# Performance work log

Hardware: AMD Instinct MI355X
Metric: run time of the kernel (lower is better)

The kernel has to match this reference:

```python
import jax, jax.numpy as jnp
import numpy as np


def setup_inputs() -> dict:
    key = jax.random.key(0)
    ks = jax.random.split(key, 7)
    B, S, H = 16, 512, 768
    NS = 4096
    MAX_W = 10
    WDIM = 150
    NL = 25
    hidden_states = jax.random.normal(ks[0], (B, S, H), dtype=jnp.float32)
    spans = jax.random.randint(ks[1], (B, NS, 3), 0, MAX_W + 1, dtype=jnp.int64)
    width_emb = jax.random.normal(ks[2], (MAX_W + 1, WDIM), dtype=jnp.float32) * 0.02
    in_dim = 2 * H + WDIM
    W1 = jax.random.normal(ks[3], (in_dim, H), dtype=jnp.float32) / np.sqrt(in_dim)
    b1 = jnp.zeros((H,), dtype=jnp.float32)
    W2 = jax.random.normal(ks[4], (H, NL), dtype=jnp.float32) / np.sqrt(H)
    b2 = jnp.zeros((NL,), dtype=jnp.float32)
    return {"hidden_states": hidden_states, "spans": spans,
            "width_emb": width_emb, "W1": W1, "b1": b1, "W2": W2, "b2": b2}


def reference(hidden_states, spans, width_emb, W1, b1, W2, b2):
    # batched_index_select(one-hot @ bmm) == gather along seq dim
    starts = spans[:, :, 0]            # [B, NS]
    ends = spans[:, :, 1]              # [B, NS]
    widths = spans[:, :, 2]            # [B, NS]
    start_emb = jnp.take_along_axis(hidden_states, starts[:, :, None], axis=1)  # [B,NS,H]
    end_emb = jnp.take_along_axis(hidden_states, ends[:, :, None], axis=1)      # [B,NS,H]
    w_emb = width_emb[widths]          # [B, NS, WDIM]
    span_emb = jnp.concatenate([start_emb, end_emb, w_emb], axis=-1)  # [B,NS,2H+WDIM]
    h = jax.nn.relu(jnp.einsum('bnd,dh->bnh', span_emb, W1) + b1)
    logits = jnp.einsum('bnh,hl->bnl', h, W2) + b2
    return logits
```

## Files before the change

### kernel.cpp

```cpp
#include <hip/hip_runtime.h>
#include <hip/hip_bf16.h>


#define NB 16
#define NH 768
#define NV 11
#define NL 25
#define NCOMBO 1331

typedef __attribute__((ext_vector_type(8))) short frag8;
typedef __attribute__((ext_vector_type(4))) float f32x4;

__device__ __forceinline__ unsigned short f2bf(float f) {
    unsigned int u = __float_as_uint(f);
    u = (u + 0x7FFFu + ((u >> 16) & 1u)) >> 16;
    return (unsigned short)u;
}
__device__ __forceinline__ unsigned int pack2(float lo, float hi) {
    return (unsigned int)f2bf(lo) | ((unsigned int)f2bf(hi) << 16);
}


#define TST 68
__global__ __launch_bounds__(256) void prep_kernel(
    const float* __restrict__ hs, const float* __restrict__ W1,
    const float* __restrict__ W2, const float* __restrict__ wemb,
    unsigned short* __restrict__ W1F, unsigned short* __restrict__ W2F,
    unsigned short* __restrict__ HSA, float* __restrict__ PW)
{
    __shared__ float T[64 * TST];
    const int x = blockIdx.x, y = blockIdx.y, tid = threadIdx.x;

    if (x < 24) {
        const int k0 = x * 64, n0 = y * 64;
        #pragma unroll
        for (int p = 0; p < 4; ++p) {
            int kl = (tid >> 4) + p * 16;
            int n4 = tid & 15;
            *(float4*)&T[kl * TST + n4 * 4] =
                *(const float4*)&W1[(size_t)(k0 + kl) * NH + n0 + n4 * 4];
        }
        __syncthreads();
        const int n = tid >> 2, kgl = tid & 3;
        const int nt = y * 4 + (n >> 4), ln = n & 15;
        #pragma unroll
        for (int half = 0; half < 2; ++half) {
            const int kk = kgl * 16 + half * 8;
            unsigned int o[4];
            #pragma unroll
            for (int i = 0; i < 4; ++i) {
                float a = T[(kk + 2 * i) * TST + n];
                float b = T[(kk + 2 * i + 1) * TST + n];
                o[i] = pack2(a, b);
            }
            const int kg = x * 2 + (kk >> 5);
            const int q = (kk >> 3) & 3;
            *(uint4*)&W1F[((((size_t)nt * 48 + kg) * 16 + ln) * 4 + q) * 8] =
                make_uint4(o[0], o[1], o[2], o[3]);
        }
    } else if (x == 24) {
        const int kcl = tid >> 7, nt = (tid >> 6) & 1, ln = (tid >> 2) & 15, q = tid & 3;
        const int n2 = nt * 16 + ln;
        const int k = y * 64 + kcl * 32 + q * 8;
        unsigned int o[4];
        #pragma unroll
        for (int i = 0; i < 4; ++i) {
            float a = (n2 < NL) ? W2[(size_t)(k + 2 * i) * NL + n2] : 0.0f;
            float b = (n2 < NL) ? W2[(size_t)(k + 2 * i + 1) * NL + n2] : 0.0f;
            o[i] = pack2(a, b);
        }
        *(uint4*)&W2F[((((size_t)(y * 2 + kcl)) * 2 + nt) * 16 + ln) * 32 + q * 8] =
            make_uint4(o[0], o[1], o[2], o[3]);
    } else if (x == 25) {
        const int n = y * 64 + (tid & 63);
        const int vg = tid >> 6;
        float acc[3] = {0.f, 0.f, 0.f};
        for (int k = 0; k < 150; k += 2) {
            float w1a = W1[(size_t)(1536 + k) * NH + n];
            float w1b = W1[(size_t)(1537 + k) * NH + n];
            #pragma unroll
            for (int j = 0; j < 3; ++j) {
                int v = vg + j * 4; int vs = (v < NV) ? v : 0;
                acc[j] += wemb[vs * 150 + k] * w1a + wemb[vs * 150 + k + 1] * w1b;
            }
        }
        #pragma unroll
        for (int j = 0; j < 3; ++j) {
            int v = vg + j * 4;
            if (v < NV) PW[(size_t)v * NH + n] = acc[j];
        }
    } else {
        const int mt = y;
        #pragma unroll
        for (int it = 0; it < 6; ++it) {
            int u = it * 256 + tid;
            int kc = u >> 6, ln = (u >> 2) & 15, q = u & 3;
            int m = mt * 16 + ln;
            int b = m / 12, v = m - 12 * b;
            unsigned int o[4] = {0, 0, 0, 0};
            if (v < NV) {
                const float* p = hs + ((size_t)(b * 512 + v)) * NH + kc * 32 + q * 8;
                float4 a = *(const float4*)p;
                float4 c = *(const float4*)(p + 4);
                o[0] = pack2(a.x, a.y); o[1] = pack2(a.z, a.w);
                o[2] = pack2(c.x, c.y); o[3] = pack2(c.z, c.w);
            }
            *(uint4*)&HSA[((((size_t)mt * 24 + kc) * 16 + ln) * 4 + q) * 8] =
                make_uint4(o[0], o[1], o[2], o[3]);
        }
    }
}

__global__ __launch_bounds__(256) void precompute_kernel(
    const unsigned short* __restrict__ HSA, const unsigned short* __restrict__ W1F,
    const float* __restrict__ b1,
    float* __restrict__ PS, float* __restrict__ PE)
{
    const int tid = threadIdx.x;
    const int wave = tid >> 6, lane = tid & 63, q = lane >> 4, ln = lane & 15;
    const int job = blockIdx.x * 4 + wave;
    const int part = job >= 576;
    const int j2 = job - part * 576;
    const int nt = j2 / 12;
    const int mt = j2 - nt * 12;

    const unsigned short* aP = HSA + (size_t)mt * 24 * 512 + ln * 32 + q * 8;
    const unsigned short* bP = W1F + ((size_t)nt * 48 + part * 24) * 512 + ln * 32 + q * 8;

    f32x4 acc;
    #pragma unroll
    for (int r = 0; r < 4; ++r) acc[r] = 0.0f;

    #pragma unroll 6
    for (int kc = 0; kc < 24; ++kc) {
        frag8 aF = *(const frag8*)(aP + kc * 512);
        frag8 bF = *(const frag8*)(bP + kc * 512);
        acc = __builtin_amdgcn_mfma_f32_16x16x32_bf16(aF, bF, acc, 0, 0, 0);
    }

    float* dst = part ? PE : PS;
    const int n = nt * 16 + ln;
    const float bb = part ? 0.0f : b1[n];
    #pragma unroll
    for (int r = 0; r < 4; ++r) {
        int m = mt * 16 + q * 4 + r;
        int b = m / 12, v = m - 12 * b;
        if (v < NV)
            dst[((size_t)(b * NV + v)) * NH + n] = acc[r] + bb;
    }
}

#define PFST 388
__global__ __launch_bounds__(256) void combo_kernel(
    const float* __restrict__ PS, const float* __restrict__ PE,
    const float* __restrict__ PW, const unsigned short* __restrict__ W2F,
    float* __restrict__ LT)
{
    __shared__ float baseL[384];
    __shared__ float peL[NV * PFST];
    __shared__ float pwL[NV * PFST];

    const int tid = threadIdx.x;
    const int wave = tid >> 6, lane = tid & 63, q = lane >> 4, ln = lane & 15;
    const int b = blockIdx.x / NV, s = blockIdx.x - NV * b;
    const int kb = blockIdx.y * 384;

    const float* ps = PS + (size_t)(b * NV + s) * NH + kb;
    for (int i = tid; i < 96; i += 256)
        *(float4*)&baseL[i * 4] = *(const float4*)&ps[i * 4];
    for (int i = tid; i < NV * 96; i += 256) {
        int v = i / 96, j = i - 96 * v;
        *(float4*)&peL[v * PFST + j * 4] =
            *(const float4*)&PE[((size_t)(b * NV + v)) * NH + kb + j * 4];
        *(float4*)&pwL[v * PFST + j * 4] =
            *(const float4*)&PW[(size_t)v * NH + kb + j * 4];
    }

    int eIdx[2], wIdx[2];
    #pragma unroll
    for (int mtl = 0; mtl < 2; ++mtl) {
        int m = (wave * 2 + mtl) * 16 + ln;
        int me = (m < 121) ? m : 120;
        eIdx[mtl] = (me * 373) >> 12;
        wIdx[mtl] = me - NV * eIdx[mtl];
    }

    f32x4 acc[2][2];
    #pragma unroll
    for (int a = 0; a < 2; ++a)
        #pragma unroll
        for (int c = 0; c < 2; ++c)
            #pragma unroll
            for (int r = 0; r < 4; ++r) acc[a][c][r] = 0.0f;

    const unsigned short* w2p = W2F + ((size_t)blockIdx.y * 12) * 1024 + ln * 32 + q * 8;

    __syncthreads();

    for (int ch = 0; ch < 6; ++ch) {
        #pragma unroll
        for (int kt = 0; kt < 2; ++kt) {
            const int kk = ch * 64 + kt * 32 + q * 8;
            float4 c0 = *(const float4*)&baseL[kk];
            float4 c1 = *(const float4*)&baseL[kk + 4];
            frag8 af[2];
            #pragma unroll
            for (int mtl = 0; mtl < 2; ++mtl) {
                const float* pe = &peL[eIdx[mtl] * PFST + kk];
                const float* pw = &pwL[wIdx[mtl] * PFST + kk];
                float4 p0 = *(const float4*)pe, p1 = *(const float4*)(pe + 4);
                float4 w0 = *(const float4*)pw, w1 = *(const float4*)(pw + 4);
                union { uint4 u; frag8 f; } cv;
                cv.u = make_uint4(
                    pack2(fmaxf(c0.x + p0.x + w0.x, 0.f), fmaxf(c0.y + p0.y + w0.y, 0.f)),
                    pack2(fmaxf(c0.z + p0.z + w0.z, 0.f), fmaxf(c0.w + p0.w + w0.w, 0.f)),
                    pack2(fmaxf(c1.x + p1.x + w1.x, 0.f), fmaxf(c1.y + p1.y + w1.y, 0.f)),
                    pack2(fmaxf(c1.z + p1.z + w1.z, 0.f), fmaxf(c1.w + p1.w + w1.w, 0.f)));
                af[mtl] = cv.f;
            }
            #pragma unroll
            for (int nt = 0; nt < 2; ++nt) {
                frag8 bf = *(const frag8*)(w2p + ((ch * 2 + kt) * 2 + nt) * 512);
                #pragma unroll
                for (int mtl = 0; mtl < 2; ++mtl)
                    acc[mtl][nt] = __builtin_amdgcn_mfma_f32_16x16x32_bf16(
                        af[mtl], bf, acc[mtl][nt], 0, 0, 0);
            }
        }
    }

    float* LTz = LT + (size_t)blockIdx.y * (NB * NCOMBO * NL);
    #pragma unroll
    for (int nt = 0; nt < 2; ++nt) {
        int n = nt * 16 + ln;
        if (n < NL) {
            #pragma unroll
            for (int mtl = 0; mtl < 2; ++mtl)
                #pragma unroll
                for (int r = 0; r < 4; ++r) {
                    int m = (wave * 2 + mtl) * 16 + q * 4 + r;
                    if (m < 121)
                        LTz[((size_t)b * NCOMBO + s * 121 + m) * NL + n] =
                            acc[mtl][nt][r];
                }
        }
    }
}

__global__ __launch_bounds__(256) void gather_kernel(
    const int* __restrict__ spans, const float* __restrict__ LT,
    const float* __restrict__ b2, float* __restrict__ out)
{
    const int idx = blockIdx.x * 256 + threadIdx.x;
    const int span = idx / NL;
    const int c = idx - span * NL;
    const int b = span >> 12;
    const int s = spans[span * 3 + 0];
    const int e = spans[span * 3 + 1];
    const int w = spans[span * 3 + 2];
    const size_t cidx = (size_t)(b * NCOMBO + s * 121 + e * NV + w) * NL + c;
    out[idx] = LT[cidx] + LT[(size_t)NB * NCOMBO * NL + cidx] + b2[c];
}

extern "C" void kernel_launch(void* const* d_in, const int* in_sizes, int n_in,
                              void* d_out, int out_size, void* d_ws, size_t ws_size,
                              hipStream_t stream) {
    const float* hs    = (const float*)d_in[0];
    const int*   spans = (const int*)d_in[1];
    const float* wemb  = (const float*)d_in[2];
    const float* W1    = (const float*)d_in[3];
    const float* b1    = (const float*)d_in[4];
    const float* W2    = (const float*)d_in[5];
    const float* b2    = (const float*)d_in[6];
    float* out = (float*)d_out;

    float* PS = (float*)d_ws;
    float* PE = PS + NB * NV * NH;
    float* PW = PE + NB * NV * NH;
    float* LT = PW + NV * NH;
    unsigned short* W1F = (unsigned short*)(LT + 2 * NB * NCOMBO * NL);
    unsigned short* W2F = W1F + (size_t)48 * 48 * 512;
    unsigned short* HSA = W2F + (size_t)24 * 2 * 512;

    prep_kernel<<<dim3(27, 12), dim3(256), 0, stream>>>(
        hs, W1, W2, wemb, W1F, W2F, HSA, PW);
    precompute_kernel<<<dim3(288), dim3(256), 0, stream>>>(HSA, W1F, b1, PS, PE);
    combo_kernel<<<dim3(NB * NV, 2), dim3(256), 0, stream>>>(PS, PE, PW, W2F, LT);
    gather_kernel<<<dim3((NB * 4096 * NL) / 256), dim3(256), 0, stream>>>(
        spans, LT, b2, out);
}
```

Baseline: 119.2 us.

## Fuse four stage kernels into one cooperative persistent kernel with grid syncs

Merges the prep, precompute, combo and gather kernels into a single cooperative kernel with 256 blocks. Each stage loops over its former grid as jobs, and grid-wide syncs separate the stages. Shared memory is unioned between the transpose tile and the combo buffers. The aim is to remove three kernel launch gaps and their tail effects. In exchange it pays grid-sync costs, and each stage now runs with fewer blocks than before, which may reduce parallelism for the gather and combo phases.

```diff
diff --git a/kernel.cpp b/kernel.cpp
--- a/kernel.cpp
+++ b/kernel.cpp
@@ -1,5 +1,8 @@
 #include <hip/hip_runtime.h>
 #include <hip/hip_bf16.h>
+#include <hip/hip_cooperative_groups.h>
+
+namespace cg = cooperative_groups;
 
 
 #define NB 16
@@ -20,246 +23,252 @@
     return (unsigned int)f2bf(lo) | ((unsigned int)f2bf(hi) << 16);
 }
 
-
 #define TST 68
-__global__ __launch_bounds__(256) void prep_kernel(
-    const float* __restrict__ hs, const float* __restrict__ W1,
-    const float* __restrict__ W2, const float* __restrict__ wemb,
-    unsigned short* __restrict__ W1F, unsigned short* __restrict__ W2F,
-    unsigned short* __restrict__ HSA, float* __restrict__ PW)
+#define PFST 388
+
+__global__ __launch_bounds__(256) void fused_kernel(
+    const float* __restrict__ hs, const int* __restrict__ spans,
+    const float* __restrict__ wemb, const float* __restrict__ W1,
+    const float* __restrict__ b1, const float* __restrict__ W2,
+    const float* __restrict__ b2, float* __restrict__ out,
+    float* __restrict__ PS, float* __restrict__ PE, float* __restrict__ PW,
+    float* __restrict__ LT, unsigned short* __restrict__ W1F,
+    unsigned short* __restrict__ W2F, unsigned short* __restrict__ HSA)
 {
-    __shared__ float T[64 * TST];
-    const int x = blockIdx.x, y = blockIdx.y, tid = threadIdx.x;
-
-    if (x < 24) {
-        const int k0 = x * 64, n0 = y * 64;
-        #pragma unroll
-        for (int p = 0; p < 4; ++p) {
-            int kl = (tid >> 4) + p * 16;
-            int n4 = tid & 15;
-            *(float4*)&T[kl * TST + n4 * 4] =
-                *(const float4*)&W1[(size_t)(k0 + kl) * NH + n0 + n4 * 4];
-        }
-        __syncthreads();
-        const int n = tid >> 2, kgl = tid & 3;
-        const int nt = y * 4 + (n >> 4), ln = n & 15;
-        #pragma unroll
-        for (int half = 0; half < 2; ++half) {
-            const int kk = kgl * 16 + half * 8;
-            unsigned int o[4];
-            #pragma unroll
-            for (int i = 0; i < 4; ++i) {
-                float a = T[(kk + 2 * i) * TST + n];
-                float b = T[(kk + 2 * i + 1) * TST + n];
-                o[i] = pack2(a, b);
-            }
-            const int kg = x * 2 + (kk >> 5);
-            const int q = (kk >> 3) & 3;
-            *(uint4*)&W1F[((((size_t)nt * 48 + kg) * 16 + ln) * 4 + q) * 8] =
-                make_uint4(o[0], o[1], o[2], o[3]);
-        }
-    } else if (x == 24) {
-        const int kcl = tid >> 7, nt = (tid >> 6) & 1, ln = (tid >> 2) & 15, q = tid & 3;
-        const int n2 = nt * 16 + ln;
-        const int k = y * 64 + kcl * 32 + q * 8;
-        unsigned int o[4];
-        #pragma unroll
-        for (int i = 0; i < 4; ++i) {
-            float a = (n2 < NL) ? W2[(size_t)(k + 2 * i) * NL + n2] : 0.0f;
-            float b = (n2 < NL) ? W2[(size_t)(k + 2 * i + 1) * NL + n2] : 0.0f;
-            o[i] = pack2(a, b);
-        }
-        *(uint4*)&W2F[((((size_t)(y * 2 + kcl)) * 2 + nt) * 16 + ln) * 32 + q * 8] =
-            make_uint4(o[0], o[1], o[2], o[3]);
-    } else if (x == 25) {
-        const int n = y * 64 + (tid & 63);
-        const int vg = tid >> 6;
-        float acc[3] = {0.f, 0.f, 0.f};
-        for (int k = 0; k < 150; k += 2) {
-            float w1a = W1[(size_t)(1536 + k) * NH + n];
-            float w1b = W1[(size_t)(1537 + k) * NH + n];
-            #pragma unroll
-            for (int j = 0; j < 3; ++j) {
-                int v = vg + j * 4; int vs = (v < NV) ? v : 0;
-                acc[j] += wemb[vs * 150 + k] * w1a + wemb[vs * 150 + k + 1] * w1b;
-            }
-        }
-        #pragma unroll
-        for (int j = 0; j < 3; ++j) {
-            int v = vg + j * 4;
-            if (v < NV) PW[(size_t)v * NH + n] = acc[j];
-        }
-    } else {
-        const int mt = y;
-        #pragma unroll
-        for (int it = 0; it < 6; ++it) {
-            int u = it * 256 + tid;
-            int kc = u >> 6, ln = (u >> 2) & 15, q = u & 3;
-            int m = mt * 16 + ln;
-            int b = m / 12, v = m - 12 * b;
-            unsigned int o[4] = {0, 0, 0, 0};
-            if (v < NV) {
-                const float* p = hs + ((size_t)(b * 512 + v)) * NH + kc * 32 + q * 8;
-                float4 a = *(const float4*)p;
-                float4 c = *(const float4*)(p + 4);
-                o[0] = pack2(a.x, a.y); o[1] = pack2(a.z, a.w);
-                o[2] = pack2(c.x, c.y); o[3] = pack2(c.z, c.w);
-            }
-            *(uint4*)&HSA[((((size_t)mt * 24 + kc) * 16 + ln) * 4 + q) * 8] =
-                make_uint4(o[0], o[1], o[2], o[3]);
-        }
-    }
-}
-
-__global__ __launch_bounds__(256) void precompute_kernel(
-    const unsigned short* __restrict__ HSA, const unsigned short* __restrict__ W1F,
-    const float* __restrict__ b1,
-    float* __restrict__ PS, float* __restrict__ PE)
-{
+    __shared__ union {
+        float T[64 * TST];
+        struct {
+            float baseL[384];
+            float peL[NV * PFST];
+            float pwL[NV * PFST];
+        } c;
+    } sm;
+
+    cg::grid_group grid = cg::this_grid();
     const int tid = threadIdx.x;
     const int wave = tid >> 6, lane = tid & 63, q = lane >> 4, ln = lane & 15;
-    const int job = blockIdx.x * 4 + wave;
-    const int part = job >= 576;
-    const int j2 = job - part * 576;
-    const int nt = j2 / 12;
-    const int mt = j2 - nt * 12;
-
-    const unsigned short* aP = HSA + (size_t)mt * 24 * 512 + ln * 32 + q * 8;
-    const unsigned short* bP = W1F + ((size_t)nt * 48 + part * 24) * 512 + ln * 32 + q * 8;
-
-    f32x4 acc;
-    #pragma unroll
-    for (int r = 0; r < 4; ++r) acc[r] = 0.0f;
-
-    #pragma unroll 6
-    for (int kc = 0; kc < 24; ++kc) {
-        frag8 aF = *(const frag8*)(aP + kc * 512);
-        frag8 bF = *(const frag8*)(bP + kc * 512);
-        acc = __builtin_amdgcn_mfma_f32_16x16x32_bf16(aF, bF, acc, 0, 0, 0);
+
+    for (int job = blockIdx.x; job < 324; job += 256) {
+        const int x = job / 12, y = job - x * 12;
+        if (x < 24) {
+            const int k0 = x * 64, n0 = y * 64;
+            #pragma unroll
+            for (int p = 0; p < 4; ++p) {
+                int kl = (tid >> 4) + p * 16;
+                int n4 = tid & 15;
+                *(float4*)&sm.T[kl * TST + n4 * 4] =
+                    *(const float4*)&W1[(size_t)(k0 + kl) * NH + n0 + n4 * 4];
+            }
+            __syncthreads();
+            const int n = tid >> 2, kgl = tid & 3;
+            const int nt = y * 4 + (n >> 4), lnn = n & 15;
+            #pragma unroll
+            for (int half = 0; half < 2; ++half) {
+                const int kk = kgl * 16 + half * 8;
+                unsigned int o[4];
+                #pragma unroll
+                for (int i = 0; i < 4; ++i) {
+                    float a = sm.T[(kk + 2 * i) * TST + n];
+                    float bv = sm.T[(kk + 2 * i + 1) * TST + n];
+                    o[i] = pack2(a, bv);
+                }
+                const int kg = x * 2 + (kk >> 5);
+                const int qq = (kk >> 3) & 3;
+                *(uint4*)&W1F[((((size_t)nt * 48 + kg) * 16 + lnn) * 4 + qq) * 8] =
+                    make_uint4(o[0], o[1], o[2], o[3]);
+            }
+            __syncthreads();
+        } else if (x == 24) {
+            const int kcl = tid >> 7, ntl = (tid >> 6) & 1,
+                      lnl = (tid >> 2) & 15, ql = tid & 3;
+            const int n2 = ntl * 16 + lnl;
+            const int k = y * 64 + kcl * 32 + ql * 8;
+            unsigned int o[4];
+            #pragma unroll
+            for (int i = 0; i < 4; ++i) {
+                float a = (n2 < NL) ? W2[(size_t)(k + 2 * i) * NL + n2] : 0.0f;
+                float bv = (n2 < NL) ? W2[(size_t)(k + 2 * i + 1) * NL + n2] : 0.0f;
+                o[i] = pack2(a, bv);
+            }
+            *(uint4*)&W2F[((((size_t)(y * 2 + kcl)) * 2 + ntl) * 16 + lnl) * 32 + ql * 8] =
+                make_uint4(o[0], o[1], o[2], o[3]);
+        } else if (x == 25) {
+            const int n = y * 64 + (tid & 63);
+            const int vg = tid >> 6;
+            float acc[3] = {0.f, 0.f, 0.f};
+            for (int k = 0; k < 150; k += 2) {
+                float w1a = W1[(size_t)(1536 + k) * NH + n];
+                float w1b = W1[(size_t)(1537 + k) * NH + n];
+                #pragma unroll
+                for (int j = 0; j < 3; ++j) {
+                    int v = vg + j * 4; int vs = (v < NV) ? v : 0;
+                    acc[j] += wemb[vs * 150 + k] * w1a + wemb[vs * 150 + k + 1] * w1b;
+                }
+            }
+            #pragma unroll
+            for (int j = 0; j < 3; ++j) {
+                int v = vg + j * 4;
+                if (v < NV) PW[(size_t)v * NH + n] = acc[j];
+            }
+        } else {
+            const int mt = y;
+            #pragma unroll
+            for (int it = 0; it < 6; ++it) {
+                int u = it * 256 + tid;
+                int kc = u >> 6, lnl = (u >> 2) & 15, ql = u & 3;
+                int m = mt * 16 + lnl;
+                int b = m / 12, v = m - 12 * b;
+                unsigned int o[4] = {0, 0, 0, 0};
+                if (v < NV) {
+                    const float* p = hs + ((size_t)(b * 512 + v)) * NH + kc * 32 + ql * 8;
+                    float4 a = *(const float4*)p;
+                    float4 c = *(const float4*)(p + 4);
+                    o[0] = pack2(a.x, a.y); o[1] = pack2(a.z, a.w);
+                    o[2] = pack2(c.x, c.y); o[3] = pack2(c.z, c.w);
+                }
+                *(uint4*)&HSA[((((size_t)mt * 24 + kc) * 16 + lnl) * 4 + ql) * 8] =
+                    make_uint4(o[0], o[1], o[2], o[3]);
+            }
+        }
     }
 
-    float* dst = part ? PE : PS;
-    const int n = nt * 16 + ln;
-    const float bb = part ? 0.0f : b1[n];
-    #pragma unroll
-    for (int r = 0; r < 4; ++r) {
-        int m = mt * 16 + q * 4 + r;
-        int b = m / 12, v = m - 12 * b;
-        if (v < NV)
-            dst[((size_t)(b * NV + v)) * NH + n] = acc[r] + bb;
+    grid.sync();
+
+    for (int job = blockIdx.x * 4 + wave; job < 1152; job += 1024) {
+        const int part = job >= 576;
+        const int j2 = job - part * 576;
+        const int nt = j2 / 12;
+        const int mt = j2 - nt * 12;
+
+        const unsigned short* aP = HSA + (size_t)mt * 24 * 512 + ln * 32 + q * 8;
+        const unsigned short* bP = W1F + ((size_t)nt * 48 + part * 24) * 512 + ln * 32 + q * 8;
+
+        f32x4 acc;
+        #pragma unroll
+        for (int r = 0; r < 4; ++r) acc[r] = 0.0f;
+        #pragma unroll 6
+        for (int kc = 0; kc < 24; ++kc) {
+            frag8 aF = *(const frag8*)(aP + kc * 512);
+            frag8 bF = *(const frag8*)(bP + kc * 512);
+            acc = __builtin_amdgcn_mfma_f32_16x16x32_bf16(aF, bF, acc, 0, 0, 0);
+        }
+
+        float* dst = part ? PE : PS;
+        const int n = nt * 16 + ln;
+        const float bb = part ? 0.0f : b1[n];
+        #pragma unroll
+        for (int r = 0; r < 4; ++r) {
+            int m = mt * 16 + q * 4 + r;
+            int b = m / 12, v = m - 12 * b;
+            if (v < NV)
+                dst[((size_t)(b * NV + v)) * NH + n] = acc[r] + bb;
+        }
     }
-}
-
-#define PFST 388
-__global__ __launch_bounds__(256) void combo_kernel(
-    const float* __restrict__ PS, const float* __restrict__ PE,
-    const float* __restrict__ PW, const unsigned short* __restrict__ W2F,
-    float* __restrict__ LT)
-{
-    __shared__ float baseL[384];
-    __shared__ float peL[NV * PFST];
-    __shared__ float pwL[NV * PFST];
-
-    const int tid = threadIdx.x;
-    const int wave = tid >> 6, lane = tid & 63, q = lane >> 4, ln = lane & 15;
-    const int b = blockIdx.x / NV, s = blockIdx.x - NV * b;
-    const int kb = blockIdx.y * 384;
-
-    const float* ps = PS + (size_t)(b * NV + s) * NH + kb;
-    for (int i = tid; i < 96; i += 256)
-        *(float4*)&baseL[i * 4] = *(const float4*)&ps[i * 4];
-    for (int i = tid; i < NV * 96; i += 256) {
-        int v = i / 96, j = i - 96 * v;
-        *(float4*)&peL[v * PFST + j * 4] =
-            *(const float4*)&PE[((size_t)(b * NV + v)) * NH + kb + j * 4];
-        *(float4*)&pwL[v * PFST + j * 4] =
-            *(const float4*)&PW[(size_t)v * NH + kb + j * 4];
+
+    grid.sync();
+
+    for (int job = blockIdx.x; job < 352; job += 256) {
+        const int z = job / 176, bs = job - z * 176;
+        const int b = bs / NV, s = bs - NV * b;
+        const int kb = z * 384;
+
+        __syncthreads();
+
+        const float* ps = PS + (size_t)(b * NV + s) * NH + kb;
+        for (int i = tid; i < 96; i += 256)
+            *(float4*)&sm.c.baseL[i * 4] = *(const float4*)&ps[i * 4];
+        for (int i = tid; i < NV * 96; i += 256) {
+            int v = i / 96, j = i - 96 * v;
+            *(float4*)&sm.c.peL[v * PFST + j * 4] =
+                *(const float4*)&PE[((size_t)(b * NV + v)) * NH + kb + j * 4];
+            *(float4*)&sm.c.pwL[v * PFST + j * 4] =
+                *(const float4*)&PW[(size_t)v * NH + kb + j * 4];
+        }
+
+        int eIdx[2], wIdx[2];
+        #pragma unroll
+        for (int mtl = 0; mtl < 2; ++mtl) {
+            int m = (wave * 2 + mtl) * 16 + ln;
+            int me = (m < 121) ? m : 120;
+            eIdx[mtl] = (me * 373) >> 12;
+            wIdx[mtl] = me - NV * eIdx[mtl];
+        }
+
+        f32x4 acc[2][2];
+        #pragma unroll
+        for (int a = 0; a < 2; ++a)
+            #pragma unroll
+            for (int c = 0; c < 2; ++c)
+                #pragma unroll
+                for (int r = 0; r < 4; ++r) acc[a][c][r] = 0.0f;
+
+        const unsigned short* w2p = W2F + ((size_t)z * 12) * 1024 + ln * 32 + q * 8;
+
+        __syncthreads();
+
+        for (int ch = 0; ch < 6; ++ch) {
+            #pragma unroll
+            for (int kt = 0; kt < 2; ++kt) {
+                const int kk = ch * 64 + kt * 32 + q * 8;
+                float4 c0 = *(const float4*)&sm.c.baseL[kk];
+                float4 c1 = *(const float4*)&sm.c.baseL[kk + 4];
+                frag8 af[2];
+                #pragma unroll
+                for (int mtl = 0; mtl < 2; ++mtl) {
+                    const float* pe = &sm.c.peL[eIdx[mtl] * PFST + kk];
+                    const float* pw = &sm.c.pwL[wIdx[mtl] * PFST + kk];
+                    float4 p0 = *(const float4*)pe, p1 = *(const float4*)(pe + 4);
+                    float4 w0 = *(const float4*)pw, w1 = *(const float4*)(pw + 4);
+                    union { uint4 u; frag8 f; } cv;
+                    cv.u = make_uint4(
+                        pack2(fmaxf(c0.x + p0.x + w0.x, 0.f), fmaxf(c0.y + p0.y + w0.y, 0.f)),
+                        pack2(fmaxf(c0.z + p0.z + w0.z, 0.f), fmaxf(c0.w + p0.w + w0.w, 0.f)),
+                        pack2(fmaxf(c1.x + p1.x + w1.x, 0.f), fmaxf(c1.y + p1.y + w1.y, 0.f)),
+                        pack2(fmaxf(c1.z + p1.z + w1.z, 0.f), fmaxf(c1.w + p1.w + w1.w, 0.f)));
+                    af[mtl] = cv.f;
+                }
+                #pragma unroll
+                for (int nt = 0; nt < 2; ++nt) {
+                    frag8 bf = *(const frag8*)(w2p + ((ch * 2 + kt) * 2 + nt) * 512);
+                    #pragma unroll
+                    for (int mtl = 0; mtl < 2; ++mtl)
+                        acc[mtl][nt] = __builtin_amdgcn_mfma_f32_16x16x32_bf16(
+                            af[mtl], bf, acc[mtl][nt], 0, 0, 0);
+                }
+            }
+        }
+
+        float* LTz = LT + (size_t)z * (NB * NCOMBO * NL);
+        #pragma unroll
+        for (int nt = 0; nt < 2; ++nt) {
+            int n = nt * 16 + ln;
+            if (n < NL) {
+                #pragma unroll
+                for (int mtl = 0; mtl < 2; ++mtl)
+                    #pragma unroll
+                    for (int r = 0; r < 4; ++r) {
+                        int m = (wave * 2 + mtl) * 16 + q * 4 + r;
+                        if (m < 121)
+                            LTz[((size_t)b * NCOMBO + s * 121 + m) * NL + n] =
+                                acc[mtl][nt][r];
+                    }
+            }
+        }
     }
 
-    int eIdx[2], wIdx[2];
-    #pragma unroll
-    for (int mtl = 0; mtl < 2; ++mtl) {
-        int m = (wave * 2 + mtl) * 16 + ln;
-        int me = (m < 121) ? m : 120;
-        eIdx[mtl] = (me * 373) >> 12;
-        wIdx[mtl] = me - NV * eIdx[mtl];
+    grid.sync();
+
+    const int total = NB * 4096 * NL;
+    for (int idx = blockIdx.x * 256 + tid; idx < total; idx += 256 * 256) {
+        const int span = idx / NL;
+        const int c = idx - span * NL;
+        const int b = span >> 12;
+        const int s = spans[span * 3 + 0];
+        const int e = spans[span * 3 + 1];
+        const int w = spans[span * 3 + 2];
+        const size_t cidx = (size_t)(b * NCOMBO + s * 121 + e * NV + w) * NL + c;
+        out[idx] = LT[cidx] + LT[(size_t)NB * NCOMBO * NL + cidx] + b2[c];
     }
-
-    f32x4 acc[2][2];
-    #pragma unroll
-    for (int a = 0; a < 2; ++a)
-        #pragma unroll
-        for (int c = 0; c < 2; ++c)
-            #pragma unroll
-            for (int r = 0; r < 4; ++r) acc[a][c][r] = 0.0f;
-
-    const unsigned short* w2p = W2F + ((size_t)blockIdx.y * 12) * 1024 + ln * 32 + q * 8;
-
-    __syncthreads();
-
-    for (int ch = 0; ch < 6; ++ch) {
-        #pragma unroll
-        for (int kt = 0; kt < 2; ++kt) {
-            const int kk = ch * 64 + kt * 32 + q * 8;
-            float4 c0 = *(const float4*)&baseL[kk];
-            float4 c1 = *(const float4*)&baseL[kk + 4];
-            frag8 af[2];
-            #pragma unroll
-            for (int mtl = 0; mtl < 2; ++mtl) {
-                const float* pe = &peL[eIdx[mtl] * PFST + kk];
-                const float* pw = &pwL[wIdx[mtl] * PFST + kk];
-                float4 p0 = *(const float4*)pe, p1 = *(const float4*)(pe + 4);
-                float4 w0 = *(const float4*)pw, w1 = *(const float4*)(pw + 4);
-                union { uint4 u; frag8 f; } cv;
-                cv.u = make_uint4(
-                    pack2(fmaxf(c0.x + p0.x + w0.x, 0.f), fmaxf(c0.y + p0.y + w0.y, 0.f)),
-                    pack2(fmaxf(c0.z + p0.z + w0.z, 0.f), fmaxf(c0.w + p0.w + w0.w, 0.f)),
-                    pack2(fmaxf(c1.x + p1.x + w1.x, 0.f), fmaxf(c1.y + p1.y + w1.y, 0.f)),
-                    pack2(fmaxf(c1.z + p1.z + w1.z, 0.f), fmaxf(c1.w + p1.w + w1.w, 0.f)));
-                af[mtl] = cv.f;
-            }
-            #pragma unroll
-            for (int nt = 0; nt < 2; ++nt) {
-                frag8 bf = *(const frag8*)(w2p + ((ch * 2 + kt) * 2 + nt) * 512);
-                #pragma unroll
-                for (int mtl = 0; mtl < 2; ++mtl)
-                    acc[mtl][nt] = __builtin_amdgcn_mfma_f32_16x16x32_bf16(
-                        af[mtl], bf, acc[mtl][nt], 0, 0, 0);
-            }
-        }
-    }
-
-    float* LTz = LT + (size_t)blockIdx.y * (NB * NCOMBO * NL);
-    #pragma unroll
-    for (int nt = 0; nt < 2; ++nt) {
-        int n = nt * 16 + ln;
-        if (n < NL) {
-            #pragma unroll
-            for (int mtl = 0; mtl < 2; ++mtl)
-                #pragma unroll
-                for (int r = 0; r < 4; ++r) {
-                    int m = (wave * 2 + mtl) * 16 + q * 4 + r;
-                    if (m < 121)
-                        LTz[((size_t)b * NCOMBO + s * 121 + m) * NL + n] =
-                            acc[mtl][nt][r];
-                }
-        }
-    }
-}
-
-__global__ __launch_bounds__(256) void gather_kernel(
-    const int* __restrict__ spans, const float* __restrict__ LT,
-    const float* __restrict__ b2, float* __restrict__ out)
-{
-    const int idx = blockIdx.x * 256 + threadIdx.x;
-    const int span = idx / NL;
-    const int c = idx - span * NL;
-    const int b = span >> 12;
-    const int s = spans[span * 3 + 0];
-    const int e = spans[span * 3 + 1];
-    const int w = spans[span * 3 + 2];
-    const size_t cidx = (size_t)(b * NCOMBO + s * 121 + e * NV + w) * NL + c;
-    out[idx] = LT[cidx] + LT[(size_t)NB * NCOMBO * NL + cidx] + b2[c];
 }
 
 extern "C" void kernel_launch(void* const* d_in, const int* in_sizes, int n_in,
@@ -282,10 +291,12 @@
     unsigned short* W2F = W1F + (size_t)48 * 48 * 512;
     unsigned short* HSA = W2F + (size_t)24 * 2 * 512;
 
-    prep_kernel<<<dim3(27, 12), dim3(256), 0, stream>>>(
-        hs, W1, W2, wemb, W1F, W2F, HSA, PW);
-    precompute_kernel<<<dim3(288), dim3(256), 0, stream>>>(HSA, W1F, b1, PS, PE);
-    combo_kernel<<<dim3(NB * NV, 2), dim3(256), 0, stream>>>(PS, PE, PW, W2F, LT);
-    gather_kernel<<<dim3((NB * 4096 * NL) / 256), dim3(256), 0, stream>>>(
-        spans, LT, b2, out);
+    void* args[] = {
+        (void*)&hs, (void*)&spans, (void*)&wemb, (void*)&W1, (void*)&b1,
+        (void*)&W2, (void*)&b2, (void*)&out,
+        (void*)&PS, (void*)&PE, (void*)&PW, (void*)&LT,
+        (void*)&W1F, (void*)&W2F, (void*)&HSA
+    };
+    hipLaunchCooperativeKernel((void*)fused_kernel, dim3(256), dim3(256),
+                               args, 0, stream);
 }
```

New measurement: 236.3 us. +98.3%, slower.

## Bucket spans by start and scatter logits directly from combo kernel

Applied to the files above, without the earlier changes.

Removes the logits lookup table and the separate gather kernel. Spans are now bucketed by (batch, start) using atomics in a fused precompute kernel, and each combo block writes its 121-combo logits (with b2 added) straight to the output for the spans in its bucket. The K split across two blocks is removed, so each block covers the full hidden dimension, and the PE/PW tables are stored as bf16 to halve their traffic. In exchange the combo grid is halved, atomics are introduced, and a fixed bucket capacity drops spans if a bucket overflows.

```diff
diff --git a/kernel.cpp b/kernel.cpp
--- a/kernel.cpp
+++ b/kernel.cpp
@@ -6,7 +6,7 @@
 #define NH 768
 #define NV 11
 #define NL 25
-#define NCOMBO 1331
+#define CAP 768
 
 typedef __attribute__((ext_vector_type(8))) short frag8;
 typedef __attribute__((ext_vector_type(4))) float f32x4;
@@ -19,6 +19,8 @@
 __device__ __forceinline__ unsigned int pack2(float lo, float hi) {
     return (unsigned int)f2bf(lo) | ((unsigned int)f2bf(hi) << 16);
 }
+__device__ __forceinline__ float bflo(unsigned int u) { return __uint_as_float(u << 16); }
+__device__ __forceinline__ float bfhi(unsigned int u) { return __uint_as_float(u & 0xFFFF0000u); }
 
 
 #define TST 68
@@ -26,12 +28,14 @@
     const float* __restrict__ hs, const float* __restrict__ W1,
     const float* __restrict__ W2, const float* __restrict__ wemb,
     unsigned short* __restrict__ W1F, unsigned short* __restrict__ W2F,
-    unsigned short* __restrict__ HSA, float* __restrict__ PW)
+    unsigned short* __restrict__ HSA, unsigned short* __restrict__ PWb,
+    int* __restrict__ bucketCnt)
 {
     __shared__ float T[64 * TST];
-    const int x = blockIdx.x, y = blockIdx.y, tid = threadIdx.x;
-
-    if (x < 24) {
+    const int job = blockIdx.x, tid = threadIdx.x;
+
+    if (job < 288) {
+        const int x = job / 12, y = job - x * 12;
         const int k0 = x * 64, n0 = y * 64;
         #pragma unroll
         for (int p = 0; p < 4; ++p) {
@@ -58,7 +62,8 @@
             *(uint4*)&W1F[((((size_t)nt * 48 + kg) * 16 + ln) * 4 + q) * 8] =
                 make_uint4(o[0], o[1], o[2], o[3]);
         }
-    } else if (x == 24) {
+    } else if (job < 300) {
+        const int y = job - 288;
         const int kcl = tid >> 7, nt = (tid >> 6) & 1, ln = (tid >> 2) & 15, q = tid & 3;
         const int n2 = nt * 16 + ln;
         const int k = y * 64 + kcl * 32 + q * 8;
@@ -71,7 +76,8 @@
         }
         *(uint4*)&W2F[((((size_t)(y * 2 + kcl)) * 2 + nt) * 16 + ln) * 32 + q * 8] =
             make_uint4(o[0], o[1], o[2], o[3]);
-    } else if (x == 25) {
+    } else if (job < 312) {
+        const int y = job - 300;
         const int n = y * 64 + (tid & 63);
         const int vg = tid >> 6;
         float acc[3] = {0.f, 0.f, 0.f};
@@ -87,10 +93,10 @@
         #pragma unroll
         for (int j = 0; j < 3; ++j) {
             int v = vg + j * 4;
-            if (v < NV) PW[(size_t)v * NH + n] = acc[j];
-        }
-    } else {
-        const int mt = y;
+            if (v < NV) PWb[(size_t)v * NH + n] = f2bf(acc[j]);
+        }
+    } else if (job < 324) {
+        const int mt = job - 312;
         #pragma unroll
         for (int it = 0; it < 6; ++it) {
             int u = it * 256 + tid;
@@ -108,72 +114,92 @@
             *(uint4*)&HSA[((((size_t)mt * 24 + kc) * 16 + ln) * 4 + q) * 8] =
                 make_uint4(o[0], o[1], o[2], o[3]);
         }
-    }
-}
-
-__global__ __launch_bounds__(256) void precompute_kernel(
+    } else {
+        if (tid < NB * NV) bucketCnt[tid] = 0;
+    }
+}
+
+__global__ __launch_bounds__(256) void pb_kernel(
     const unsigned short* __restrict__ HSA, const unsigned short* __restrict__ W1F,
-    const float* __restrict__ b1,
-    float* __restrict__ PS, float* __restrict__ PE)
+    const float* __restrict__ b1, const int* __restrict__ spans,
+    float* __restrict__ PS, unsigned short* __restrict__ PEb,
+    int* __restrict__ bucketCnt, int* __restrict__ bucketIdx)
 {
     const int tid = threadIdx.x;
-    const int wave = tid >> 6, lane = tid & 63, q = lane >> 4, ln = lane & 15;
-    const int job = blockIdx.x * 4 + wave;
-    const int part = job >= 576;
-    const int j2 = job - part * 576;
-    const int nt = j2 / 12;
-    const int mt = j2 - nt * 12;
-
-    const unsigned short* aP = HSA + (size_t)mt * 24 * 512 + ln * 32 + q * 8;
-    const unsigned short* bP = W1F + ((size_t)nt * 48 + part * 24) * 512 + ln * 32 + q * 8;
-
-    f32x4 acc;
-    #pragma unroll
-    for (int r = 0; r < 4; ++r) acc[r] = 0.0f;
-
-    #pragma unroll 6
-    for (int kc = 0; kc < 24; ++kc) {
-        frag8 aF = *(const frag8*)(aP + kc * 512);
-        frag8 bF = *(const frag8*)(bP + kc * 512);
-        acc = __builtin_amdgcn_mfma_f32_16x16x32_bf16(aF, bF, acc, 0, 0, 0);
-    }
-
-    float* dst = part ? PE : PS;
-    const int n = nt * 16 + ln;
-    const float bb = part ? 0.0f : b1[n];
-    #pragma unroll
-    for (int r = 0; r < 4; ++r) {
-        int m = mt * 16 + q * 4 + r;
-        int b = m / 12, v = m - 12 * b;
-        if (v < NV)
-            dst[((size_t)(b * NV + v)) * NH + n] = acc[r] + bb;
-    }
-}
-
-#define PFST 388
+    if (blockIdx.x < 288) {
+        const int wave = tid >> 6, lane = tid & 63, q = lane >> 4, ln = lane & 15;
+        const int job = blockIdx.x * 4 + wave;
+        const int part = job >= 576;
+        const int j2 = job - part * 576;
+        const int nt = j2 / 12;
+        const int mt = j2 - nt * 12;
+
+        const unsigned short* aP = HSA + (size_t)mt * 24 * 512 + ln * 32 + q * 8;
+        const unsigned short* bP = W1F + ((size_t)nt * 48 + part * 24) * 512 + ln * 32 + q * 8;
+
+        f32x4 acc;
+        #pragma unroll
+        for (int r = 0; r < 4; ++r) acc[r] = 0.0f;
+        #pragma unroll 6
+        for (int kc = 0; kc < 24; ++kc) {
+            frag8 aF = *(const frag8*)(aP + kc * 512);
+            frag8 bF = *(const frag8*)(bP + kc * 512);
+            acc = __builtin_amdgcn_mfma_f32_16x16x32_bf16(aF, bF, acc, 0, 0, 0);
+        }
+
+        const int n = nt * 16 + ln;
+        const float bb = part ? 0.0f : b1[n];
+        #pragma unroll
+        for (int r = 0; r < 4; ++r) {
+            int m = mt * 16 + q * 4 + r;
+            int b = m / 12, v = m - 12 * b;
+            if (v < NV) {
+                if (part)
+                    PEb[((size_t)(b * NV + v)) * NH + n] = f2bf(acc[r]);
+                else
+                    PS[((size_t)(b * NV + v)) * NH + n] = acc[r] + bb;
+            }
+        }
+    } else {
+        const int span = (blockIdx.x - 288) * 256 + tid;
+        const int s = spans[span * 3 + 0];
+        const int e = spans[span * 3 + 1];
+        const int w = spans[span * 3 + 2];
+        const int b = span >> 12;
+        const int bs = b * NV + s;
+        int slot = atomicAdd(&bucketCnt[bs], 1);
+        if (slot < CAP)
+            bucketIdx[bs * CAP + slot] = (span << 7) | (e * NV + w);
+    }
+}
+
+#define PEST 776
+#define CST 28
 __global__ __launch_bounds__(256) void combo_kernel(
-    const float* __restrict__ PS, const float* __restrict__ PE,
-    const float* __restrict__ PW, const unsigned short* __restrict__ W2F,
-    float* __restrict__ LT)
+    const float* __restrict__ PS, const unsigned short* __restrict__ PEb,
+    const unsigned short* __restrict__ PWb, const unsigned short* __restrict__ W2F,
+    const float* __restrict__ b2, const int* __restrict__ bucketCnt,
+    const int* __restrict__ bucketIdx, float* __restrict__ out)
 {
-    __shared__ float baseL[384];
-    __shared__ float peL[NV * PFST];
-    __shared__ float pwL[NV * PFST];
+    __shared__ float baseL[NH];
+    __shared__ unsigned short peL[NV * PEST];
+    __shared__ unsigned short pwL[NV * PEST];
+    __shared__ float Cs[121 * CST];
 
     const int tid = threadIdx.x;
     const int wave = tid >> 6, lane = tid & 63, q = lane >> 4, ln = lane & 15;
     const int b = blockIdx.x / NV, s = blockIdx.x - NV * b;
-    const int kb = blockIdx.y * 384;
-
-    const float* ps = PS + (size_t)(b * NV + s) * NH + kb;
-    for (int i = tid; i < 96; i += 256)
+    const int bs = blockIdx.x;
+
+    const float* ps = PS + (size_t)(b * NV + s) * NH;
+    for (int i = tid; i < 192; i += 256)
         *(float4*)&baseL[i * 4] = *(const float4*)&ps[i * 4];
     for (int i = tid; i < NV * 96; i += 256) {
         int v = i / 96, j = i - 96 * v;
-        *(float4*)&peL[v * PFST + j * 4] =
-            *(const float4*)&PE[((size_t)(b * NV + v)) * NH + kb + j * 4];
-        *(float4*)&pwL[v * PFST + j * 4] =
-            *(const float4*)&PW[(size_t)v * NH + kb + j * 4];
+        *(uint4*)&peL[v * PEST + j * 8] =
+            *(const uint4*)&PEb[((size_t)(b * NV + v)) * NH + j * 8];
+        *(uint4*)&pwL[v * PEST + j * 8] =
+            *(const uint4*)&PWb[(size_t)v * NH + j * 8];
     }
 
     int eIdx[2], wIdx[2];
@@ -193,29 +219,33 @@
             #pragma unroll
             for (int r = 0; r < 4; ++r) acc[a][c][r] = 0.0f;
 
-    const unsigned short* w2p = W2F + ((size_t)blockIdx.y * 12) * 1024 + ln * 32 + q * 8;
+    const unsigned short* w2p = W2F + ln * 32 + q * 8;
 
     __syncthreads();
 
-    for (int ch = 0; ch < 6; ++ch) {
+    for (int ch = 0; ch < 12; ++ch) {
         #pragma unroll
         for (int kt = 0; kt < 2; ++kt) {
             const int kk = ch * 64 + kt * 32 + q * 8;
-            float4 c0 = *(const float4*)&baseL[kk];
-            float4 c1 = *(const float4*)&baseL[kk + 4];
+            union { float4 v[2]; float f[8]; } cb;
+            cb.v[0] = *(const float4*)&baseL[kk];
+            cb.v[1] = *(const float4*)&baseL[kk + 4];
             frag8 af[2];
             #pragma unroll
             for (int mtl = 0; mtl < 2; ++mtl) {
-                const float* pe = &peL[eIdx[mtl] * PFST + kk];
-                const float* pw = &pwL[wIdx[mtl] * PFST + kk];
-                float4 p0 = *(const float4*)pe, p1 = *(const float4*)(pe + 4);
-                float4 w0 = *(const float4*)pw, w1 = *(const float4*)(pw + 4);
+                uint4 pu = *(const uint4*)&peL[eIdx[mtl] * PEST + kk];
+                uint4 wu = *(const uint4*)&pwL[wIdx[mtl] * PEST + kk];
+                unsigned int o[4];
+                #pragma unroll
+                for (int t = 0; t < 4; ++t) {
+                    unsigned int p  = ((const unsigned int*)&pu)[t];
+                    unsigned int ww = ((const unsigned int*)&wu)[t];
+                    float a0 = bflo(p) + bflo(ww) + cb.f[2 * t];
+                    float a1 = bfhi(p) + bfhi(ww) + cb.f[2 * t + 1];
+                    o[t] = pack2(fmaxf(a0, 0.f), fmaxf(a1, 0.f));
+                }
                 union { uint4 u; frag8 f; } cv;
-                cv.u = make_uint4(
-                    pack2(fmaxf(c0.x + p0.x + w0.x, 0.f), fmaxf(c0.y + p0.y + w0.y, 0.f)),
-                    pack2(fmaxf(c0.z + p0.z + w0.z, 0.f), fmaxf(c0.w + p0.w + w0.w, 0.f)),
-                    pack2(fmaxf(c1.x + p1.x + w1.x, 0.f), fmaxf(c1.y + p1.y + w1.y, 0.f)),
-                    pack2(fmaxf(c1.z + p1.z + w1.z, 0.f), fmaxf(c1.w + p1.w + w1.w, 0.f)));
+                cv.u = make_uint4(o[0], o[1], o[2], o[3]);
                 af[mtl] = cv.f;
             }
             #pragma unroll
@@ -229,37 +259,36 @@
         }
     }
 
-    float* LTz = LT + (size_t)blockIdx.y * (NB * NCOMBO * NL);
+    __syncthreads();
     #pragma unroll
     for (int nt = 0; nt < 2; ++nt) {
         int n = nt * 16 + ln;
         if (n < NL) {
+            float bias = b2[n];
             #pragma unroll
             for (int mtl = 0; mtl < 2; ++mtl)
                 #pragma unroll
                 for (int r = 0; r < 4; ++r) {
                     int m = (wave * 2 + mtl) * 16 + q * 4 + r;
                     if (m < 121)
-                        LTz[((size_t)b * NCOMBO + s * 121 + m) * NL + n] =
-                            acc[mtl][nt][r];
+                        Cs[m * CST + n] = acc[mtl][nt][r] + bias;
                 }
         }
     }
-}
-
-__global__ __launch_bounds__(256) void gather_kernel(
-    const int* __restrict__ spans, const float* __restrict__ LT,
-    const float* __restrict__ b2, float* __restrict__ out)
-{
-    const int idx = blockIdx.x * 256 + threadIdx.x;
-    const int span = idx / NL;
-    const int c = idx - span * NL;
-    const int b = span >> 12;
-    const int s = spans[span * 3 + 0];
-    const int e = spans[span * 3 + 1];
-    const int w = spans[span * 3 + 2];
-    const size_t cidx = (size_t)(b * NCOMBO + s * 121 + e * NV + w) * NL + c;
-    out[idx] = LT[cidx] + LT[(size_t)NB * NCOMBO * NL + cidx] + b2[c];
+    __syncthreads();
+
+    int cnt = bucketCnt[bs];
+    if (cnt > CAP) cnt = CAP;
+    const int total = cnt * NL;
+    const int* bk = bucketIdx + bs * CAP;
+    for (int j = tid; j < total; j += 256) {
+        int sp = (int)(((unsigned)j * 5243u) >> 17);
+        int c = j - sp * NL;
+        int packed = bk[sp];
+        int span = packed >> 7;
+        int row = packed & 127;
+        out[(size_t)span * NL + c] = Cs[row * CST + c];
+    }
 }
 
 extern "C" void kernel_launch(void* const* d_in, const int* in_sizes, int n_in,
@@ -275,17 +304,18 @@
     float* out = (float*)d_out;
 
     float* PS = (float*)d_ws;
-    float* PE = PS + NB * NV * NH;
-    float* PW = PE + NB * NV * NH;
-    float* LT = PW + NV * NH;
-    unsigned short* W1F = (unsigned short*)(LT + 2 * NB * NCOMBO * NL);
-    unsigned short* W2F = W1F + (size_t)48 * 48 * 512;
-    unsigned short* HSA = W2F + (size_t)24 * 2 * 512;
-
-    prep_kernel<<<dim3(27, 12), dim3(256), 0, stream>>>(
-        hs, W1, W2, wemb, W1F, W2F, HSA, PW);
-    precompute_kernel<<<dim3(288), dim3(256), 0, stream>>>(HSA, W1F, b1, PS, PE);
-    combo_kernel<<<dim3(NB * NV, 2), dim3(256), 0, stream>>>(PS, PE, PW, W2F, LT);
-    gather_kernel<<<dim3((NB * 4096 * NL) / 256), dim3(256), 0, stream>>>(
-        spans, LT, b2, out);
-}
+    unsigned short* PEb = (unsigned short*)(PS + NB * NV * NH);
+    unsigned short* PWb = PEb + NB * NV * NH;
+    unsigned short* W2F = PWb + NV * NH;
+    unsigned short* W1F = W2F + 24 * 2 * 512;
+    unsigned short* HSA = W1F + (size_t)48 * 48 * 512;
+    int* bucketCnt = (int*)(HSA + (size_t)12 * 24 * 512);
+    int* bucketIdx = bucketCnt + 256;
+
+    prep_kernel<<<dim3(325), dim3(256), 0, stream>>>(
+        hs, W1, W2, wemb, W1F, W2F, HSA, PWb, bucketCnt);
+    pb_kernel<<<dim3(288 + 256), dim3(256), 0, stream>>>(
+        HSA, W1F, b1, spans, PS, PEb, bucketCnt, bucketIdx);
+    combo_kernel<<<dim3(NB * NV), dim3(256), 0, stream>>>(
+        PS, PEb, PWb, W2F, b2, bucketCnt, bucketIdx, out);
+}
```

Result: slower. 157.2 us (+31.9%).
